# Optimization experiments

Measured on AMD Instinct MI355X. Metric: run time of the kernel, lower is better.

## Reference

```python
import jax, jax.numpy as jnp
import numpy as np


def setup_inputs() -> dict:
    key = jax.random.key(0)
    k1, k2, k3, k4 = jax.random.split(key, 4)
    B, T, d_model, d_internal = 4, 2048, 1024, 64
    x = jax.random.normal(k1, (B, T, d_model), dtype=jnp.float32)
    # torch.nn.Linear weights: [out_features, in_features]
    s = 1.0 / np.sqrt(d_model)
    W_Q = jax.random.uniform(k2, (d_internal, d_model), jnp.float32, -s, s)
    W_K = jax.random.uniform(k3, (d_internal, d_model), jnp.float32, -s, s)
    W_V = jax.random.uniform(k4, (d_internal, d_model), jnp.float32, -s, s)
    return {"x": x, "W_Q": W_Q, "W_K": W_K, "W_V": W_V}


def reference(x, W_Q, W_K, W_V):
    B, T, C = x.shape  # C == d_model
    Q = jnp.einsum('btc,dc->btd', x, W_Q)
    K = jnp.einsum('btc,dc->btd', x, W_K)
    # Faithful to source bug: V is computed with W_K, W_V is unused.
    V = jnp.einsum('btc,dc->btd', x, W_K)
    scale = C ** (-0.5)  # source scales by d_model, not d_internal
    attn = jnp.einsum('btd,bsd->bts', Q, K) * scale  # [B,T,T]
    causal = jnp.tril(jnp.ones((T, T), dtype=bool))
    attn = jnp.where(causal[None, :, :], attn, -jnp.inf)
    attn = jax.nn.softmax(attn, axis=-1)
    return jnp.einsum('bts,bsd->btd', attn, V)
```

## Files before the change

kernel.cpp:

```cpp
#include <hip/hip_runtime.h>
#include <hip/hip_bf16.h>
#include <cstdint>
#include <cstddef>

#define BB 4
#define TT 2048
#define DM 1024
#define DH 64

typedef __attribute__((ext_vector_type(8))) short short8;
typedef __attribute__((ext_vector_type(4))) float floatx4;

__device__ __forceinline__ unsigned short f2bf(float f) {
    union { float f; unsigned int u; } v; v.f = f;
    unsigned int u = v.u;
    u += 0x7fffu + ((u >> 16) & 1u);
    return (unsigned short)(u >> 16);
}

__global__ __launch_bounds__(256) void wconv_kernel(const float* __restrict__ wq,
                                                    const float* __restrict__ wk,
                                                    unsigned short* __restrict__ wb) {
    int i = blockIdx.x * 256 + threadIdx.x;
    const float* src = (i < 16384) ? (wq + (size_t)i * 4)
                                   : (wk + (size_t)(i - 16384) * 4);
    float4 v = *reinterpret_cast<const float4*>(src);
    ushort4 o;
    o.x = f2bf(v.x); o.y = f2bf(v.y); o.z = f2bf(v.z); o.w = f2bf(v.w);
    *reinterpret_cast<ushort4*>(wb + (size_t)i * 4) = o;
}

__global__ __launch_bounds__(128) void proj_kernel(const float* __restrict__ x,
                                                   const unsigned short* __restrict__ wb,
                                                   unsigned short* __restrict__ qo,
                                                   unsigned short* __restrict__ ko,
                                                   unsigned short* __restrict__ kt) {
    const int tid  = threadIdx.x;
    const int wave = tid >> 6;
    const int lane = tid & 63;
    const int col  = lane & 15;
    const int quad = lane >> 4;
    const int m0   = blockIdx.x * 16;

    floatx4 acc[4];
#pragma unroll
    for (int i = 0; i < 4; ++i) acc[i] = (floatx4){0.f, 0.f, 0.f, 0.f};

    const float* xp = x + (size_t)(m0 + col) * DM + quad * 8;
    const unsigned short* wp = wb + (size_t)(wave * 64) * DM;

#pragma unroll 2
    for (int k0 = 0; k0 < DM; k0 += 32) {
        float4 xa = *reinterpret_cast<const float4*>(xp + k0);
        float4 xb = *reinterpret_cast<const float4*>(xp + k0 + 4);
        short8 a;
        a[0] = (short)f2bf(xa.x); a[1] = (short)f2bf(xa.y);
        a[2] = (short)f2bf(xa.z); a[3] = (short)f2bf(xa.w);
        a[4] = (short)f2bf(xb.x); a[5] = (short)f2bf(xb.y);
        a[6] = (short)f2bf(xb.z); a[7] = (short)f2bf(xb.w);
#pragma unroll
        for (int nt = 0; nt < 4; ++nt) {
            short8 b = *reinterpret_cast<const short8*>(
                wp + (size_t)(nt * 16 + col) * DM + k0 + quad * 8);
            acc[nt] = __builtin_amdgcn_mfma_f32_16x16x32_bf16(a, b, acc[nt], 0, 0, 0);
        }
    }

#pragma unroll
    for (int nt = 0; nt < 4; ++nt) {
        const int n = nt * 16 + col;
#pragma unroll
        for (int r = 0; r < 4; ++r) {
            const size_t row = (size_t)(m0 + quad * 4 + r);
            float v = acc[nt][r];
            if (wave == 0) {
                qo[row * DH + n] = f2bf(v * 0.03125f);
            } else {
                unsigned short h = f2bf(v);
                ko[row * DH + n] = h;
                const int b = (int)(row >> 11);
                const int s = (int)(row & 2047);
                kt[((size_t)(b * 64 + n)) * TT + s] = h;
            }
        }
    }
}

__global__ __launch_bounds__(128) void flash1_kernel(const unsigned short* __restrict__ qb,
                                                     const unsigned short* __restrict__ kb,
                                                     const unsigned short* __restrict__ ktb,
                                                     float* __restrict__ Op,
                                                     float* __restrict__ ml) {
    const int c  = blockIdx.x & 7;
    const int qt = (blockIdx.x >> 3) & 63;
    const int b  = blockIdx.x >> 9;
    if (8 * c > qt) return;

    __shared__ __align__(16) unsigned short Pl[2][16][32];

    const int tid  = threadIdx.x;
    const int wave = tid >> 6;
    const int lane = tid & 63;
    const int col  = lane & 15;
    const int quad = lane >> 4;

    const int q0    = qt * 32;
    const int qrow  = q0 + wave * 16;
    const int s_beg = c * 256;
    const int s_end = min(s_beg + 256, q0 + 32);

    const unsigned short* qp  = qb  + ((size_t)b * TT + qrow) * DH;
    const unsigned short* kp  = kb  + (size_t)b * TT * DH;
    const unsigned short* ktp = ktb + (size_t)b * 64 * TT;

    short8 qf0 = *reinterpret_cast<const short8*>(qp + (size_t)col * DH + quad * 8);
    short8 qf1 = *reinterpret_cast<const short8*>(qp + (size_t)col * DH + 32 + quad * 8);

    floatx4 o[4];
#pragma unroll
    for (int t = 0; t < 4; ++t) o[t] = (floatx4){0.f, 0.f, 0.f, 0.f};
    float mrow[4], lrow[4];
    int   myq[4];
#pragma unroll
    for (int r = 0; r < 4; ++r) {
        mrow[r] = -INFINITY; lrow[r] = 0.f;
        myq[r] = qrow + quad * 4 + r;
    }
    const float LOG2E = 1.44269504f;

    for (int s0 = s_beg; s0 < s_end; s0 += 32) {
        float sv[2][4];
        float mtile[4];
#pragma unroll
        for (int r = 0; r < 4; ++r) mtile[r] = -INFINITY;
#pragma unroll
        for (int st = 0; st < 2; ++st) {
            const unsigned short* kr = kp + (size_t)(s0 + st * 16 + col) * DH + quad * 8;
            short8 kf0 = *reinterpret_cast<const short8*>(kr);
            short8 kf1 = *reinterpret_cast<const short8*>(kr + 32);
            floatx4 z = (floatx4){0.f, 0.f, 0.f, 0.f};
            z = __builtin_amdgcn_mfma_f32_16x16x32_bf16(qf0, kf0, z, 0, 0, 0);
            z = __builtin_amdgcn_mfma_f32_16x16x32_bf16(qf1, kf1, z, 0, 0, 0);
            const int skey = s0 + st * 16 + col;
#pragma unroll
            for (int r = 0; r < 4; ++r) {
                float v = z[r] * LOG2E;
                v = (skey <= myq[r]) ? v : -INFINITY;
                sv[st][r] = v;
                mtile[r] = fmaxf(mtile[r], v);
            }
        }
#pragma unroll
        for (int m = 1; m < 16; m <<= 1)
#pragma unroll
            for (int r = 0; r < 4; ++r)
                mtile[r] = fmaxf(mtile[r], __shfl_xor(mtile[r], m, 64));

        float alpha[4], rsum[4];
#pragma unroll
        for (int r = 0; r < 4; ++r) {
            float mnew = fmaxf(mrow[r], mtile[r]);
            alpha[r] = exp2f(mrow[r] - mnew);
            mrow[r] = mnew;
            float p0 = exp2f(sv[0][r] - mnew);
            float p1 = exp2f(sv[1][r] - mnew);
            sv[0][r] = p0; sv[1][r] = p1;
            rsum[r] = p0 + p1;
        }
#pragma unroll
        for (int m = 1; m < 16; m <<= 1)
#pragma unroll
            for (int r = 0; r < 4; ++r)
                rsum[r] += __shfl_xor(rsum[r], m, 64);
#pragma unroll
        for (int r = 0; r < 4; ++r) lrow[r] = lrow[r] * alpha[r] + rsum[r];
#pragma unroll
        for (int t = 0; t < 4; ++t)
#pragma unroll
            for (int r = 0; r < 4; ++r)
                o[t][r] *= alpha[r];

#pragma unroll
        for (int st = 0; st < 2; ++st)
#pragma unroll
            for (int r = 0; r < 4; ++r)
                Pl[wave][quad * 4 + r][st * 16 + col] = f2bf(sv[st][r]);
        short8 pf = *reinterpret_cast<const short8*>(&Pl[wave][col][quad * 8]);

#pragma unroll
        for (int t = 0; t < 4; ++t) {
            short8 vf = *reinterpret_cast<const short8*>(
                ktp + (size_t)(t * 16 + col) * TT + s0 + quad * 8);
            o[t] = __builtin_amdgcn_mfma_f32_16x16x32_bf16(pf, vf, o[t], 0, 0, 0);
        }
    }

    const int slot = (b * 64 + qt) * 8 + c;
    float* op = Op + (size_t)slot * 2048;
#pragma unroll
    for (int t = 0; t < 4; ++t)
#pragma unroll
        for (int r = 0; r < 4; ++r)
            op[(size_t)(wave * 16 + quad * 4 + r) * DH + t * 16 + col] = o[t][r];
    if (col == 0) {
        float* mlp = ml + (size_t)slot * 64;
#pragma unroll
        for (int r = 0; r < 4; ++r) {
            mlp[wave * 16 + quad * 4 + r]      = mrow[r];
            mlp[32 + wave * 16 + quad * 4 + r] = lrow[r];
        }
    }
}

__global__ __launch_bounds__(256) void merge_kernel(const float* __restrict__ Op,
                                                    const float* __restrict__ ml,
                                                    float* __restrict__ out) {
    const int qt  = blockIdx.x & 63;
    const int b   = blockIdx.x >> 6;
    const int nch = (qt >> 3) + 1;
    const int t   = threadIdx.x;
    const int row = t >> 3;
    const int c8  = (t & 7) * 8;
    const size_t base = (size_t)blockIdx.x * 8;

    float M = -INFINITY;
    for (int c = 0; c < nch; ++c)
        M = fmaxf(M, ml[(base + c) * 64 + row]);

    float L = 0.f;
    float a[8];
#pragma unroll
    for (int i = 0; i < 8; ++i) a[i] = 0.f;
    for (int c = 0; c < nch; ++c) {
        const float m_c = ml[(base + c) * 64 + row];
        const float l_c = ml[(base + c) * 64 + 32 + row];
        const float w = exp2f(m_c - M);
        L += l_c * w;
        const float* op = Op + (base + c) * 2048 + (size_t)row * 64 + c8;
        float4 v0 = *reinterpret_cast<const float4*>(op);
        float4 v1 = *reinterpret_cast<const float4*>(op + 4);
        a[0] += w * v0.x; a[1] += w * v0.y; a[2] += w * v0.z; a[3] += w * v0.w;
        a[4] += w * v1.x; a[5] += w * v1.y; a[6] += w * v1.z; a[7] += w * v1.w;
    }
    const float inv = 1.0f / L;
    float* o = out + ((size_t)b * TT + qt * 32 + row) * DH + c8;
    float4 r0 = {a[0] * inv, a[1] * inv, a[2] * inv, a[3] * inv};
    float4 r1 = {a[4] * inv, a[5] * inv, a[6] * inv, a[7] * inv};
    *reinterpret_cast<float4*>(o)     = r0;
    *reinterpret_cast<float4*>(o + 4) = r1;
}

extern "C" void kernel_launch(void* const* d_in, const int* in_sizes, int n_in,
                              void* d_out, int out_size, void* d_ws, size_t ws_size,
                              hipStream_t stream) {
    const float* x  = (const float*)d_in[0];
    const float* wq = (const float*)d_in[1];
    const float* wk = (const float*)d_in[2];

    unsigned short* qo = (unsigned short*)d_ws;
    unsigned short* ko = qo + (size_t)BB * TT * DH;
    unsigned short* wb = ko + (size_t)BB * TT * DH;
    unsigned short* kt = wb + (size_t)128 * DM;
    float* Op = (float*)(kt + (size_t)BB * DH * TT);
    float* ml = Op + (size_t)2048 * 2048;
    float* out = (float*)d_out;

    hipLaunchKernelGGL(wconv_kernel,  dim3(128),            dim3(256), 0, stream, wq, wk, wb);
    hipLaunchKernelGGL(proj_kernel,   dim3((BB * TT) / 16), dim3(128), 0, stream, x, wb, qo, ko, kt);
    hipLaunchKernelGGL(flash1_kernel, dim3(BB * 64 * 8),    dim3(128), 0, stream, qo, ko, kt, Op, ml);
    hipLaunchKernelGGL(merge_kernel,  dim3(BB * 64),        dim3(256), 0, stream, Op, ml, out);
}
```

Measured before the change: 137.7 us.

## Pre-convert x to bf16, widen projection waves, and halve flash KV chunk size

Converts x to bf16 in a separate conversion pass alongside the weights. The projection kernel now runs four waves, each computing 32 output columns instead of 64, to raise parallelism and register headroom. The flash kernel splits keys into 128-wide chunks instead of 256, doubling the number of blocks for better load balance over the causal triangle, and the merge kernel combines more partials. This adds a full fp32-read/bf16-write pass over x and larger partial-output buffers in exchange.

```diff
diff --git a/kernel.cpp b/kernel.cpp
--- a/kernel.cpp
+++ b/kernel.cpp
@@ -18,19 +18,32 @@
     return (unsigned short)(u >> 16);
 }
 
-__global__ __launch_bounds__(256) void wconv_kernel(const float* __restrict__ wq,
-                                                    const float* __restrict__ wk,
-                                                    unsigned short* __restrict__ wb) {
+#define XQUADS (BB * TT * DM / 4)
+#define WQUADS (DH * DM / 4)
+
+__global__ __launch_bounds__(256) void conv_kernel(const float* __restrict__ x,
+                                                   const float* __restrict__ wq,
+                                                   const float* __restrict__ wk,
+                                                   unsigned short* __restrict__ xb,
+                                                   unsigned short* __restrict__ wb) {
     int i = blockIdx.x * 256 + threadIdx.x;
-    const float* src = (i < 16384) ? (wq + (size_t)i * 4)
-                                   : (wk + (size_t)(i - 16384) * 4);
+    const float* src;
+    unsigned short* dst;
+    if (i < XQUADS) {
+        src = x + (size_t)i * 4;
+        dst = xb + (size_t)i * 4;
+    } else {
+        int j = i - XQUADS;
+        src = (j < WQUADS) ? (wq + (size_t)j * 4) : (wk + (size_t)(j - WQUADS) * 4);
+        dst = wb + (size_t)j * 4;
+    }
     float4 v = *reinterpret_cast<const float4*>(src);
     ushort4 o;
     o.x = f2bf(v.x); o.y = f2bf(v.y); o.z = f2bf(v.z); o.w = f2bf(v.w);
-    *reinterpret_cast<ushort4*>(wb + (size_t)i * 4) = o;
-}
-
-__global__ __launch_bounds__(128) void proj_kernel(const float* __restrict__ x,
+    *reinterpret_cast<ushort4*>(dst) = o;
+}
+
+__global__ __launch_bounds__(256) void proj_kernel(const unsigned short* __restrict__ xb,
                                                    const unsigned short* __restrict__ wb,
                                                    unsigned short* __restrict__ qo,
                                                    unsigned short* __restrict__ ko,
@@ -41,42 +54,37 @@
     const int col  = lane & 15;
     const int quad = lane >> 4;
     const int m0   = blockIdx.x * 16;
-
-    floatx4 acc[4];
-#pragma unroll
-    for (int i = 0; i < 4; ++i) acc[i] = (floatx4){0.f, 0.f, 0.f, 0.f};
-
-    const float* xp = x + (size_t)(m0 + col) * DM + quad * 8;
-    const unsigned short* wp = wb + (size_t)(wave * 64) * DM;
-
-#pragma unroll 2
+    const int gc0  = wave * 32;
+
+    floatx4 acc0 = (floatx4){0.f, 0.f, 0.f, 0.f};
+    floatx4 acc1 = (floatx4){0.f, 0.f, 0.f, 0.f};
+
+    const unsigned short* xp  = xb + (size_t)(m0 + col) * DM + quad * 8;
+    const unsigned short* wp0 = wb + (size_t)(gc0 + col) * DM + quad * 8;
+    const unsigned short* wp1 = wp0 + (size_t)16 * DM;
+
+#pragma unroll 4
     for (int k0 = 0; k0 < DM; k0 += 32) {
-        float4 xa = *reinterpret_cast<const float4*>(xp + k0);
-        float4 xb = *reinterpret_cast<const float4*>(xp + k0 + 4);
-        short8 a;
-        a[0] = (short)f2bf(xa.x); a[1] = (short)f2bf(xa.y);
-        a[2] = (short)f2bf(xa.z); a[3] = (short)f2bf(xa.w);
-        a[4] = (short)f2bf(xb.x); a[5] = (short)f2bf(xb.y);
-        a[6] = (short)f2bf(xb.z); a[7] = (short)f2bf(xb.w);
-#pragma unroll
-        for (int nt = 0; nt < 4; ++nt) {
-            short8 b = *reinterpret_cast<const short8*>(
-                wp + (size_t)(nt * 16 + col) * DM + k0 + quad * 8);
-            acc[nt] = __builtin_amdgcn_mfma_f32_16x16x32_bf16(a, b, acc[nt], 0, 0, 0);
-        }
-    }
-
-#pragma unroll
-    for (int nt = 0; nt < 4; ++nt) {
-        const int n = nt * 16 + col;
+        short8 a  = *reinterpret_cast<const short8*>(xp  + k0);
+        short8 b0 = *reinterpret_cast<const short8*>(wp0 + k0);
+        short8 b1 = *reinterpret_cast<const short8*>(wp1 + k0);
+        acc0 = __builtin_amdgcn_mfma_f32_16x16x32_bf16(a, b0, acc0, 0, 0, 0);
+        acc1 = __builtin_amdgcn_mfma_f32_16x16x32_bf16(a, b1, acc1, 0, 0, 0);
+    }
+
+#pragma unroll
+    for (int nt = 0; nt < 2; ++nt) {
+        const int g = gc0 + nt * 16 + col;
+        const floatx4& acc = nt ? acc1 : acc0;
 #pragma unroll
         for (int r = 0; r < 4; ++r) {
             const size_t row = (size_t)(m0 + quad * 4 + r);
-            float v = acc[nt][r];
-            if (wave == 0) {
-                qo[row * DH + n] = f2bf(v * 0.03125f);
+            float v = acc[r];
+            if (g < 64) {
+                qo[row * DH + g] = f2bf(v * 0.03125f);
             } else {
                 unsigned short h = f2bf(v);
+                const int n = g - 64;
                 ko[row * DH + n] = h;
                 const int b = (int)(row >> 11);
                 const int s = (int)(row & 2047);
@@ -91,10 +99,10 @@
                                                      const unsigned short* __restrict__ ktb,
                                                      float* __restrict__ Op,
                                                      float* __restrict__ ml) {
-    const int c  = blockIdx.x & 7;
-    const int qt = (blockIdx.x >> 3) & 63;
-    const int b  = blockIdx.x >> 9;
-    if (8 * c > qt) return;
+    const int c  = blockIdx.x & 15;
+    const int qt = (blockIdx.x >> 4) & 63;
+    const int b  = blockIdx.x >> 10;
+    if (4 * c > qt) return;
 
     __shared__ __align__(16) unsigned short Pl[2][16][32];
 
@@ -106,8 +114,8 @@
 
     const int q0    = qt * 32;
     const int qrow  = q0 + wave * 16;
-    const int s_beg = c * 256;
-    const int s_end = min(s_beg + 256, q0 + 32);
+    const int s_beg = c * 128;
+    const int s_end = min(s_beg + 128, q0 + 32);
 
     const unsigned short* qp  = qb  + ((size_t)b * TT + qrow) * DH;
     const unsigned short* kp  = kb  + (size_t)b * TT * DH;
@@ -195,7 +203,7 @@
         }
     }
 
-    const int slot = (b * 64 + qt) * 8 + c;
+    const int slot = (b * 64 + qt) * 16 + c;
     float* op = Op + (size_t)slot * 2048;
 #pragma unroll
     for (int t = 0; t < 4; ++t)
@@ -217,11 +225,11 @@
                                                     float* __restrict__ out) {
     const int qt  = blockIdx.x & 63;
     const int b   = blockIdx.x >> 6;
-    const int nch = (qt >> 3) + 1;
+    const int nch = (qt >> 2) + 1;
     const int t   = threadIdx.x;
     const int row = t >> 3;
     const int c8  = (t & 7) * 8;
-    const size_t base = (size_t)blockIdx.x * 8;
+    const size_t base = (size_t)blockIdx.x * 16;
 
     float M = -INFINITY;
     for (int c = 0; c < nch; ++c)
@@ -257,16 +265,18 @@
     const float* wq = (const float*)d_in[1];
     const float* wk = (const float*)d_in[2];
 
-    unsigned short* qo = (unsigned short*)d_ws;
+    unsigned short* xb = (unsigned short*)d_ws;
+    unsigned short* qo = xb + (size_t)BB * TT * DM;
     unsigned short* ko = qo + (size_t)BB * TT * DH;
     unsigned short* wb = ko + (size_t)BB * TT * DH;
     unsigned short* kt = wb + (size_t)128 * DM;
     float* Op = (float*)(kt + (size_t)BB * DH * TT);
-    float* ml = Op + (size_t)2048 * 2048;
+    float* ml = Op + (size_t)4096 * 2048;
     float* out = (float*)d_out;
 
-    hipLaunchKernelGGL(wconv_kernel,  dim3(128),            dim3(256), 0, stream, wq, wk, wb);
-    hipLaunchKernelGGL(proj_kernel,   dim3((BB * TT) / 16), dim3(128), 0, stream, x, wb, qo, ko, kt);
-    hipLaunchKernelGGL(flash1_kernel, dim3(BB * 64 * 8),    dim3(128), 0, stream, qo, ko, kt, Op, ml);
-    hipLaunchKernelGGL(merge_kernel,  dim3(BB * 64),        dim3(256), 0, stream, Op, ml, out);
-}
+    const int conv_blocks = (XQUADS + 2 * WQUADS + 255) / 256;
+    hipLaunchKernelGGL(conv_kernel,   dim3(conv_blocks),     dim3(256), 0, stream, x, wq, wk, xb, wb);
+    hipLaunchKernelGGL(proj_kernel,   dim3((BB * TT) / 16),  dim3(256), 0, stream, xb, wb, qo, ko, kt);
+    hipLaunchKernelGGL(flash1_kernel, dim3(BB * 64 * 16),    dim3(128), 0, stream, qo, ko, kt, Op, ml);
+    hipLaunchKernelGGL(merge_kernel,  dim3(BB * 64),         dim3(256), 0, stream, Op, ml, out);
+}
```

New measurement: 147.2 us. +6.9%, slower.
